# Kernel tuning notes

Measured on AMD Instinct MI355X. Metric: run time of the kernel, lower is better.

Reference implementation:

```python
import jax, jax.numpy as jnp
import numpy as np

BN_EPS = 1e-5
NEG = -9e15
ALPHA = 0.2  # LeakyReLU slope


def _gat(src, tgt, adj_mask, W, a, num_heads):
    # src: [M, H*D] source features, tgt: [N, H*D], adj_mask: [N, M] (>0 means edge)
    N, M = tgt.shape[0], src.shape[0]
    D = tgt.shape[1] // num_heads
    S = (src @ W.T).reshape(M, num_heads, D)   # W(source)
    T = (tgt @ W.T).reshape(N, num_heads, D)   # W(target)
    # concat([t_i, s_j]) . a[h] == t_i . a[h,:D] + s_j . a[h,D:]
    et = jnp.einsum('nhd,hd->hn', T, a[:, :D])  # [H, N]
    es = jnp.einsum('mhd,hd->hm', S, a[:, D:])  # [H, M]
    e = et[:, :, None] + es[:, None, :]          # [H, N, M]
    e = jnp.where(e >= 0, e, ALPHA * e)          # LeakyReLU
    e = jnp.where(adj_mask[None, :, :] > 0, e, NEG)
    attn = jax.nn.softmax(e, axis=-1)            # over source nodes
    out = jnp.einsum('hnm,mhd->nhd', attn, S)    # [N, H, D]
    return out.reshape(N, num_heads * D)


def _bn_eval(x, gamma, beta):
    # eval-mode BatchNorm1d with running_mean=0, running_var=1
    return x * (gamma / jnp.sqrt(1.0 + BN_EPS)) + beta


def setup_inputs() -> dict:
    key = jax.random.key(0)
    ks = jax.random.split(key, 12)
    N, M, H, HD = 4096, 2048, 8, 256
    D = HD // H
    c_features = jax.random.normal(ks[0], (N, HD), dtype=jnp.float32)
    d_features = jax.random.normal(ks[1], (M, HD), dtype=jnp.float32)
    cd_adj = jax.random.randint(ks[2], (N, M), 0, 2, dtype=jnp.int32)
    sc = 1.0 / np.sqrt(HD)
    c_W = jax.random.normal(ks[3], (HD, HD), dtype=jnp.float32) * sc
    d_W = jax.random.normal(ks[4], (HD, HD), dtype=jnp.float32) * sc
    sa = np.sqrt(2.0 / (H + 2 * D))  # xavier_normal_ for [H, 2D]
    c_a = jax.random.normal(ks[5], (H, 2 * D), dtype=jnp.float32) * sa
    d_a = jax.random.normal(ks[6], (H, 2 * D), dtype=jnp.float32) * sa
    c_bn_gamma = jnp.ones((HD,), dtype=jnp.float32)
    c_bn_beta = jnp.zeros((HD,), dtype=jnp.float32)
    d_bn_gamma = jnp.ones((HD,), dtype=jnp.float32)
    d_bn_beta = jnp.zeros((HD,), dtype=jnp.float32)
    return dict(c_features=c_features, d_features=d_features, cd_adj=cd_adj,
                c_W=c_W, c_a=c_a, d_W=d_W, d_a=d_a,
                c_bn_gamma=c_bn_gamma, c_bn_beta=c_bn_beta,
                d_bn_gamma=d_bn_gamma, d_bn_beta=d_bn_beta)


def reference(c_features, d_features, cd_adj, c_W, c_a, d_W, d_a,
              c_bn_gamma, c_bn_beta, d_bn_gamma, d_bn_beta):
    H = 8
    c_out = _gat(d_features, c_features, cd_adj, c_W, c_a, H)
    d_out = _gat(c_features, d_features, cd_adj.T, d_W, d_a, H)
    c_out = jax.nn.relu(_bn_eval(c_out, c_bn_gamma, c_bn_beta))
    d_out = jax.nn.relu(_bn_eval(d_out, d_bn_gamma, d_bn_beta))
    # dropout is identity in eval mode
    return (c_out, d_out)
```

## Files before the change

### kernel.cpp

```cpp
#include <hip/hip_runtime.h>
#include <hip/hip_bf16.h>

#define L2E 1.4426950408889634f
#define BNF 0.99999500003749969f

typedef __attribute__((ext_vector_type(4))) float f4;
typedef __attribute__((ext_vector_type(4))) float f32x4;
typedef __attribute__((ext_vector_type(4))) int i4;
typedef __attribute__((ext_vector_type(8))) short bfrag;

__device__ __forceinline__ int cvtpk(float lo, float hi) {
  int r;
  asm("v_cvt_pk_bf16_f32 %0, %1, %2" : "=v"(r) : "v"(lo), "v"(hi));
  return r;
}

#define MFMA16(a, b, c) __builtin_amdgcn_mfma_f32_16x16x32_bf16(a, b, c, 0, 0, 0)

__global__ __launch_bounds__(256) void prep1(
    const float* __restrict__ c_feat, const float* __restrict__ d_feat,
    const float* __restrict__ c_W, const float* __restrict__ d_W,
    const float* __restrict__ c_a, const float* __restrict__ d_a,
    const int* __restrict__ adj,
    unsigned* __restrict__ adjP, unsigned* __restrict__ adjPT,
    unsigned short* __restrict__ Xb_c, unsigned short* __restrict__ Xb_d,
    unsigned short* __restrict__ Wb_c, unsigned short* __restrict__ Wb_d,
    float* __restrict__ wa_c, float* __restrict__ wa_d) {
  const int b = blockIdx.x;
  const int t = threadIdx.x;
  if (b < 2048) {
    __shared__ int s[64][65];
    const int m0 = (b & 31) * 64, n0 = (b >> 5) * 64;
#pragma unroll
    for (int i = 0; i < 4; ++i) {
      int idx = t + i * 256;
      int r = idx >> 4, c4 = (idx & 15) * 4;
      i4 v = __builtin_nontemporal_load(
          (const i4*)(adj + (size_t)(n0 + r) * 2048 + m0 + c4));
      s[r][c4 + 0] = v.x; s[r][c4 + 1] = v.y;
      s[r][c4 + 2] = v.z; s[r][c4 + 3] = v.w;
    }
    __syncthreads();
    const int w = t >> 6, l = t & 63;
#pragma unroll 4
    for (int rr = 0; rr < 16; ++rr) {
      int r = w * 16 + rr;
      int n = n0 + r;
      unsigned long long bb = __ballot(s[r][l] != 0);
      if (l == 0) {
        size_t base = ((size_t)(n >> 4) * 64 + (m0 >> 5)) * 16 + (n & 15);
        adjP[base] = (unsigned)bb;
        adjP[base + 16] = (unsigned)(bb >> 32);
      }
    }
#pragma unroll 4
    for (int cc = 0; cc < 16; ++cc) {
      int m = m0 + w * 16 + cc;
      unsigned long long bb = __ballot(s[l][w * 16 + cc] != 0);
      if (l == 0) {
        size_t base = ((size_t)(m >> 4) * 128 + (n0 >> 5)) * 16 + (m & 15);
        adjPT[base] = (unsigned)bb;
        adjPT[base + 16] = (unsigned)(bb >> 32);
      }
    }
  } else if (b < 2880) {
    int idx = (b - 2048) * 256 + t;
    const float* S; unsigned short* D; int tt;
    if (idx < 65536)       { S = d_feat; D = Xb_c; tt = idx; }
    else if (idx < 196608) { S = c_feat; D = Xb_d; tt = idx - 65536; }
    else if (idx < 204800) { S = c_W;    D = Wb_c; tt = idx - 196608; }
    else                   { S = d_W;    D = Wb_d; tt = idx - 204800; }
    int l = tt & 63, kt = (tt >> 6) & 7, tile = tt >> 9;
    int row = tile * 16 + (l & 15);
    int col = kt * 32 + (l >> 4) * 8;
    const float* sp = S + (size_t)row * 256 + col;
    f4 v0 = *(const f4*)sp;
    f4 v1 = *(const f4*)(sp + 4);
    uint4 u;
    u.x = (unsigned)cvtpk(v0.x, v0.y);
    u.y = (unsigned)cvtpk(v0.z, v0.w);
    u.z = (unsigned)cvtpk(v1.x, v1.y);
    u.w = (unsigned)cvtpk(v1.z, v1.w);
    *(uint4*)(D + (size_t)tt * 8) = u;
  } else {
    int idx = (b - 2880) * 256 + t;
    bool cs = idx < 2048;
    int i2 = idx & 2047;
    int h = i2 >> 8, k = i2 & 255;
    const float* W = cs ? c_W : d_W;
    const float* a = cs ? c_a : d_a;
    float s = 0.f;
#pragma unroll 8
    for (int d = 0; d < 32; ++d)
      s = fmaf(a[h * 64 + d], W[(size_t)(h * 32 + d) * 256 + k], s);
    (cs ? wa_c : wa_d)[i2] = s * L2E;
  }
}

__global__ __launch_bounds__(64) void gemm2(
    const unsigned short* __restrict__ Xb_c, const unsigned short* __restrict__ Wb_c,
    const unsigned short* __restrict__ Xb_d, const unsigned short* __restrict__ Wb_d,
    const float* __restrict__ c_a, const float* __restrict__ d_a,
    unsigned short* __restrict__ Sbt_c, unsigned short* __restrict__ Sbt_d,
    float* __restrict__ es2t_c, float* __restrict__ es2t_d,
    const float* __restrict__ c_feat, const float* __restrict__ d_feat,
    const float* __restrict__ wa_c, const float* __restrict__ wa_d,
    float* __restrict__ et2_c, float* __restrict__ et2_d) {
  const int b = blockIdx.x;
  if (b < 768) {
    const bool cs = b < 256;
    const int bb = cs ? b : b - 256;
    const int rt = bb >> 1, half = bb & 1;
    const unsigned short* Xb = cs ? Xb_c : Xb_d;
    const unsigned short* Wb = cs ? Wb_c : Wb_d;
    const float* av = cs ? c_a : d_a;
    unsigned short* Sbt = cs ? Sbt_c : Sbt_d;
    float* es2t = cs ? es2t_c : es2t_d;
    const int Mrows = cs ? 2048 : 4096;
    const int l = threadIdx.x;
    const int g = l >> 4, c16 = l & 15;
    bfrag afr[8];
#pragma unroll
    for (int kt = 0; kt < 8; ++kt)
      afr[kt] = *(const bfrag*)(Xb + ((size_t)(rt * 8 + kt) * 64 + l) * 8);
    float esacc[4] = {};
#pragma unroll
    for (int c8 = 0; c8 < 8; ++c8) {
      const int cht = half * 8 + c8;
      f32x4 acc = {0.f, 0.f, 0.f, 0.f};
#pragma unroll
      for (int kt = 0; kt < 8; ++kt) {
        bfrag wfr = *(const bfrag*)(Wb + ((size_t)(cht * 8 + kt) * 64 + l) * 8);
        acc = MFMA16(afr[kt], wfr, acc);
      }
      const int mtb = rt * 2 + (g >> 1);
      size_t soff = (((size_t)cht * (Mrows >> 3) + mtb) * 16 + c16) * 8 + (g & 1) * 4;
      uint2 u;
      u.x = (unsigned)cvtpk(acc[0], acc[1]);
      u.y = (unsigned)cvtpk(acc[2], acc[3]);
      *(uint2*)(Sbt + soff) = u;
      const int h = cht >> 1, sub = cht & 1;
      const float aw = av[h * 64 + 32 + sub * 16 + c16];
      if (sub == 0) {
#pragma unroll
        for (int i = 0; i < 4; ++i) esacc[i] = acc[i] * aw;
      } else {
#pragma unroll
        for (int i = 0; i < 4; ++i) esacc[i] = fmaf(acc[i], aw, esacc[i]);
#pragma unroll
        for (int i = 0; i < 4; ++i) {
          esacc[i] += __shfl_xor(esacc[i], 1);
          esacc[i] += __shfl_xor(esacc[i], 2);
          esacc[i] += __shfl_xor(esacc[i], 4);
          esacc[i] += __shfl_xor(esacc[i], 8);
        }
        if (c16 == 0) {
          f4 o = {esacc[0] * L2E, esacc[1] * L2E, esacc[2] * L2E, esacc[3] * L2E};
          *(f4*)(es2t + (size_t)h * Mrows + rt * 16 + g * 4) = o;
        }
      }
    }
  } else {
    int idx = (b - 768) * 64 + threadIdx.x;
    bool cs = idx < 32768;
    int i2 = cs ? idx : idx - 32768;
    const float* X = cs ? c_feat : d_feat;
    const float* wa = cs ? wa_c : wa_d;
    float* et2 = cs ? et2_c : et2_d;
    int r = i2 >> 3, h = i2 & 7;
    const float* xp = X + (size_t)r * 256;
    const float* ap = wa + h * 256;
    float s = 0.f;
#pragma unroll 16
    for (int k = 0; k < 256; k += 4) {
      f4 xv = *(const f4*)(xp + k);
      f4 av = *(const f4*)(ap + k);
      s = fmaf(xv.x, av.x, s); s = fmaf(xv.y, av.y, s);
      s = fmaf(xv.z, av.z, s); s = fmaf(xv.w, av.w, s);
    }
    et2[i2] = s;
  }
}

__device__ __forceinline__ bfrag make_pfrag2(float et, f4 e0, f4 e1,
                                             unsigned bits) {
  float xv[8] = {e0.x, e0.y, e0.z, e0.w, e1.x, e1.y, e1.z, e1.w};
  float p[8];
#pragma unroll
  for (int e = 0; e < 8; ++e) {
    float x = et + xv[e];
    x = fmaxf(x, 0.2f * x);
    float pe = __builtin_amdgcn_exp2f(x);
    p[e] = ((bits >> e) & 1u) ? pe : 0.f;
  }
  union { bfrag v; int i[4]; } u;
#pragma unroll
  for (int e = 0; e < 4; ++e) u.i[e] = cvtpk(p[2 * e], p[2 * e + 1]);
  return u.v;
}

template <int FINAL, int SWZ, int CHT>
__global__ __launch_bounds__(256) void fused_attn(
    const float* __restrict__ et2_c, const float* __restrict__ es2t_c,
    const unsigned* __restrict__ adjP, const unsigned short* __restrict__ Sbt_c,
    float* __restrict__ pnum_c, float* __restrict__ pden_c,
    const float* __restrict__ et2_d, const float* __restrict__ es2t_d,
    const unsigned* __restrict__ adjPT, const unsigned short* __restrict__ Sbt_d,
    float* __restrict__ pnum_d, float* __restrict__ pden_d,
    float* __restrict__ out,
    const float* __restrict__ gc, const float* __restrict__ bc,
    const float* __restrict__ gd, const float* __restrict__ bd,
    int NBC, int CH_C, int CH_D) {
  const int b = blockIdx.x;
  bool cs; int chunk, tile;
  if (SWZ) {
    const int r = b & 7;
    if (r < 4) { cs = true;  chunk = r >> 1; tile = (b >> 3) + (r & 1) * 128; }
    else       { cs = false; chunk = r - 4;  tile = b >> 3; }
  } else {
    cs = b < NBC;
    const int bb = cs ? b : b - NBC;
    tile = cs ? (bb & 255) : (bb & 127);
    chunk = cs ? (bb >> 8) : (bb >> 7);
  }
  const int n0 = tile * 16;
  const int M = cs ? 2048 : 4096;
  const int ROWS = cs ? 4096 : 2048;
  const int CH = CHT ? CHT : (cs ? CH_C : CH_D);
  const float* et2 = cs ? et2_c : et2_d;
  const float* es2t = cs ? es2t_c : es2t_d;
  const unsigned* adjPk = cs ? adjP : adjPT;
  const unsigned short* Sbt = cs ? Sbt_c : Sbt_d;
  float* pnum = cs ? pnum_c : pnum_d;
  float* pden = cs ? pden_c : pden_d;
  const float* bng = cs ? gc : gd;
  const float* bnb = cs ? bc : bd;
  float* outp = cs ? out : out + (size_t)4096 * 256;

  const int mstart = chunk * CH;
  const int mend = mstart + CH;
  const int Mw = M >> 5;
  const int tid = threadIdx.x;
  const int w = tid >> 6, l = tid & 63;
  const int g = l >> 4, c16 = l & 15;
  const int hA = w * 2, hB = w * 2 + 1;
  const int row = n0 + c16;
  const float etA = et2[row * 8 + hA];
  const float etB = et2[row * 8 + hB];
  const int Mt16 = M * 16;
  const int lane_off = g * 128 + c16 * 8;
  const unsigned short* pA0 = Sbt + (size_t)(hA * 2) * Mt16 + lane_off;
  const unsigned short* pA1 = pA0 + Mt16;
  const unsigned short* pB0 = Sbt + (size_t)(hB * 2) * Mt16 + lane_off;
  const unsigned short* pB1 = pB0 + Mt16;
  const unsigned* adjt = adjPk + (size_t)tile * Mw * 16 + c16;
  const float* esArow = es2t + (size_t)hA * M;
  const float* esBrow = es2t + (size_t)hB * M;
  f32x4 accA0 = {0.f, 0.f, 0.f, 0.f}, accA1 = accA0, denA = accA0;
  f32x4 accB0 = accA0, accB1 = accA0, denB = accA0;
  union { bfrag v; int i[4]; } uo;
#pragma unroll
  for (int e = 0; e < 4; ++e) uo.i[e] = 0x3F803F80;
  const bfrag ones = uo.v;

  auto body = [&](int m0) {
    const unsigned w0 = adjt[(m0 >> 5) * 16];
    const unsigned w1 = adjt[(m0 >> 5) * 16 + 16];
    const int moa = m0 + g * 8;
    const int i8 = (m0 >> 3) * 128;
    f4 eA0 = *(const f4*)(esArow + moa);
    f4 eA1 = *(const f4*)(esArow + moa + 4);
    f4 eB0 = *(const f4*)(esBrow + moa);
    f4 eB1 = *(const f4*)(esBrow + moa + 4);
    f4 fA0 = *(const f4*)(esArow + moa + 32);
    f4 fA1 = *(const f4*)(esArow + moa + 36);
    f4 fB0 = *(const f4*)(esBrow + moa + 32);
    f4 fB1 = *(const f4*)(esBrow + moa + 36);
    bfrag bA0a = *(const bfrag*)(pA0 + i8);
    bfrag bA1a = *(const bfrag*)(pA1 + i8);
    bfrag bB0a = *(const bfrag*)(pB0 + i8);
    bfrag bB1a = *(const bfrag*)(pB1 + i8);
    bfrag bA0b = *(const bfrag*)(pA0 + i8 + 512);
    bfrag bA1b = *(const bfrag*)(pA1 + i8 + 512);
    bfrag bB0b = *(const bfrag*)(pB0 + i8 + 512);
    bfrag bB1b = *(const bfrag*)(pB1 + i8 + 512);
    const unsigned bits0 = (w0 >> (g * 8)) & 0xffu;
    const unsigned bits1 = (w1 >> (g * 8)) & 0xffu;
    bfrag aA = make_pfrag2(etA, eA0, eA1, bits0);
    bfrag aB = make_pfrag2(etB, eB0, eB1, bits0);
    accA0 = MFMA16(aA, bA0a, accA0);
    accA1 = MFMA16(aA, bA1a, accA1);
    denA  = MFMA16(aA, ones, denA);
    accB0 = MFMA16(aB, bB0a, accB0);
    accB1 = MFMA16(aB, bB1a, accB1);
    denB  = MFMA16(aB, ones, denB);
    bfrag cA = make_pfrag2(etA, fA0, fA1, bits1);
    bfrag cB = make_pfrag2(etB, fB0, fB1, bits1);
    accA0 = MFMA16(cA, bA0b, accA0);
    accA1 = MFMA16(cA, bA1b, accA1);
    denA  = MFMA16(cA, ones, denA);
    accB0 = MFMA16(cB, bB0b, accB0);
    accB1 = MFMA16(cB, bB1b, accB1);
    denB  = MFMA16(cB, ones, denB);
  };

  if (CHT) {
#pragma unroll 1
    for (int mm = 0; mm < CHT; mm += 512) {
#pragma unroll
      for (int it = 0; it < 8; ++it)
        body(mstart + mm + it * 64);
    }
  } else {
    for (int m0 = mstart; m0 < mend; m0 += 64)
      body(m0);
  }

#define EPILOGUE(acc0, acc1, den, h)                                          \
  {                                                                           \
    const int c0 = (h) * 32 + c16, c1 = (h) * 32 + 16 + c16;                  \
    if (FINAL) {                                                              \
      const float g0 = bng[c0] * BNF, b0 = bnb[c0];                           \
      const float g1 = bng[c1] * BNF, b1 = bnb[c1];                           \
      _Pragma("unroll") for (int i = 0; i < 4; ++i) {                         \
        float rs = 1.f / fmaxf(den[i], 1e-30f);                               \
        float* op = outp + (size_t)(n0 + g * 4 + i) * 256;                    \
        op[c0] = fmaxf(fmaf(acc0[i] * rs, g0, b0), 0.f);                      \
        op[c1] = fmaxf(fmaf(acc1[i] * rs, g1, b1), 0.f);                      \
      }                                                                       \
    } else {                                                                  \
      _Pragma("unroll") for (int i = 0; i < 4; ++i) {                         \
        size_t rr = (size_t)chunk * ROWS + n0 + g * 4 + i;                    \
        pnum[rr * 256 + c0] = acc0[i];                                        \
        pnum[rr * 256 + c1] = acc1[i];                                        \
        if (c16 == 0) pden[rr * 8 + (h)] = den[i];                            \
      }                                                                       \
    }                                                                         \
  }
  EPILOGUE(accA0, accA1, denA, hA)
  EPILOGUE(accB0, accB1, denB, hB)
#undef EPILOGUE
}

__global__ __launch_bounds__(256) void finalize_k(
    const float* __restrict__ pnum_c, const float* __restrict__ pden_c,
    const float* __restrict__ pnum_d, const float* __restrict__ pden_d,
    float* __restrict__ out,
    const float* __restrict__ gc, const float* __restrict__ bc,
    const float* __restrict__ gd, const float* __restrict__ bd,
    int cc_c, int cc_d) {
  const int b = blockIdx.x;
  const bool cs = b < 1024;
  const int idx = (cs ? b : b - 1024) * 256 + threadIdx.x;
  const int rows = cs ? 4096 : 2048;
  const int cc = cs ? cc_c : cc_d;
  const float* pnum = cs ? pnum_c : pnum_d;
  const float* pden = cs ? pden_c : pden_d;
  const float* bng = cs ? gc : gd;
  const float* bnb = cs ? bc : bd;
  float* outp = cs ? out : out + (size_t)4096 * 256;
  int r = idx >> 6, c4 = (idx & 63) * 4;
  int h = c4 >> 5;
  f4 num = {0.f, 0.f, 0.f, 0.f};
  float den = 0.f;
  for (int c = 0; c < cc; ++c) {
    size_t rr = (size_t)c * rows + r;
    num += __builtin_nontemporal_load((const f4*)(pnum + rr * 256 + c4));
    den += __builtin_nontemporal_load(pden + rr * 8 + h);
  }
  float rs = 1.f / fmaxf(den, 1e-30f);
  f4 gm = *(const f4*)(bng + c4);
  f4 bb = *(const f4*)(bnb + c4);
  f4 o;
  o.x = fmaxf(fmaf(num.x * rs, gm.x * BNF, bb.x), 0.f);
  o.y = fmaxf(fmaf(num.y * rs, gm.y * BNF, bb.y), 0.f);
  o.z = fmaxf(fmaf(num.z * rs, gm.z * BNF, bb.z), 0.f);
  o.w = fmaxf(fmaf(num.w * rs, gm.w * BNF, bb.w), 0.f);
  *(f4*)(outp + (size_t)r * 256 + c4) = o;
}

extern "C" void kernel_launch(void* const* d_in, const int* in_sizes, int n_in,
                              void* d_out, int out_size, void* d_ws, size_t ws_size,
                              hipStream_t stream) {
  const float* c_feat = (const float*)d_in[0];
  const float* d_feat = (const float*)d_in[1];
  const int*   adj    = (const int*)d_in[2];
  const float* c_W    = (const float*)d_in[3];
  const float* c_a    = (const float*)d_in[4];
  const float* d_W    = (const float*)d_in[5];
  const float* d_a    = (const float*)d_in[6];
  const float* c_bn_g = (const float*)d_in[7];
  const float* c_bn_b = (const float*)d_in[8];
  const float* d_bn_g = (const float*)d_in[9];
  const float* d_bn_b = (const float*)d_in[10];
  float* out = (float*)d_out;

  char* w = (char*)d_ws;
  size_t off = 0;
  auto take = [&](size_t bytes) -> char* {
    char* p = w + off;
    off += (bytes + 255) & ~(size_t)255;
    return p;
  };
  unsigned short* Sbt_c = (unsigned short*)take(256 * 2048 * 2);
  unsigned short* Sbt_d = (unsigned short*)take(256 * 4096 * 2);
  unsigned short* Xb_c  = (unsigned short*)take(2048 * 256 * 2);
  unsigned short* Xb_d  = (unsigned short*)take(4096 * 256 * 2);
  unsigned short* Wb_c  = (unsigned short*)take(256 * 256 * 2);
  unsigned short* Wb_d  = (unsigned short*)take(256 * 256 * 2);
  float* et2_c  = (float*)take(4096 * 8 * 4);
  float* es2t_c = (float*)take(8 * 2048 * 4);
  float* et2_d  = (float*)take(2048 * 8 * 4);
  float* es2t_d = (float*)take(8 * 4096 * 4);
  float* wa_c   = (float*)take(8 * 256 * 4);
  float* wa_d   = (float*)take(8 * 256 * 4);
  unsigned* adjP  = (unsigned*)take(4096 * 64 * 4);
  unsigned* adjPT = (unsigned*)take(2048 * 128 * 4);

  const size_t base = off;
  const size_t PC = (size_t)4096 * 256 * 4, PD = (size_t)2048 * 256 * 4;
  const size_t DC = 4096 * 8 * 4, DD = 2048 * 8 * 4;
  auto need = [&](int a, int b2) -> size_t {
    return base + (size_t)a * (PC + DC) + (size_t)b2 * (PD + DD) + 4096;
  };
  int ccc = 0, ccd = 0;
  if (ws_size >= need(2, 4))      { ccc = 2; ccd = 4; }
  else if (ws_size >= need(2, 2)) { ccc = 2; ccd = 2; }

  float* pden_c = nullptr; float* pden_d = nullptr;
  float* pnum_c = nullptr; float* pnum_d = nullptr;
  if (ccc) {
    pden_c = (float*)take((size_t)ccc * DC);
    pden_d = (float*)take((size_t)ccd * DD);
    pnum_c = (float*)take((size_t)ccc * PC);
    pnum_d = (float*)take((size_t)ccd * PD);
  }

  dim3 blk(256);
  prep1<<<2896, blk, 0, stream>>>(c_feat, d_feat, c_W, d_W, c_a, d_a, adj,
                                  adjP, adjPT, Xb_c, Xb_d, Wb_c, Wb_d,
                                  wa_c, wa_d);
  gemm2<<<1536, dim3(64), 0, stream>>>(Xb_c, Wb_c, Xb_d, Wb_d, c_a, d_a,
                                       Sbt_c, Sbt_d, es2t_c, es2t_d,
                                       c_feat, d_feat, wa_c, wa_d,
                                       et2_c, et2_d);

  if (ccc == 2 && ccd == 4) {
    fused_attn<0, 1, 1024><<<1024, blk, 0, stream>>>(
        et2_c, es2t_c, adjP, Sbt_c, pnum_c, pden_c,
        et2_d, es2t_d, adjPT, Sbt_d, pnum_d, pden_d,
        nullptr, c_bn_g, c_bn_b, d_bn_g, d_bn_b,
        512, 1024, 1024);
    finalize_k<<<1536, blk, 0, stream>>>(pnum_c, pden_c, pnum_d, pden_d, out,
                                         c_bn_g, c_bn_b, d_bn_g, d_bn_b, ccc, ccd);
  } else if (ccc) {
    fused_attn<0, 0, 0><<<256 * ccc + 128 * ccd, blk, 0, stream>>>(
        et2_c, es2t_c, adjP, Sbt_c, pnum_c, pden_c,
        et2_d, es2t_d, adjPT, Sbt_d, pnum_d, pden_d,
        nullptr, c_bn_g, c_bn_b, d_bn_g, d_bn_b,
        256 * ccc, 2048 / ccc, 4096 / ccd);
    finalize_k<<<1536, blk, 0, stream>>>(pnum_c, pden_c, pnum_d, pden_d, out,
                                         c_bn_g, c_bn_b, d_bn_g, d_bn_b, ccc, ccd);
  } else {
    fused_attn<1, 0, 0><<<384, blk, 0, stream>>>(
        et2_c, es2t_c, adjP, Sbt_c, nullptr, nullptr,
        et2_d, es2t_d, adjPT, Sbt_d, nullptr, nullptr,
        out, c_bn_g, c_bn_b, d_bn_g, d_bn_b, 256, 2048, 4096);
  }
}
```

Measured before the change: 77.99 us.

## Replace global split-M partials with in-block LDS reduction across waves

```diff
diff --git a/kernel.cpp b/kernel.cpp
--- a/kernel.cpp
+++ b/kernel.cpp
@@ -199,51 +199,35 @@
   return u.v;
 }
 
-template <int FINAL, int SWZ, int CHT>
-__global__ __launch_bounds__(256) void fused_attn(
+__global__ __launch_bounds__(256) void fused_rs(
     const float* __restrict__ et2_c, const float* __restrict__ es2t_c,
     const unsigned* __restrict__ adjP, const unsigned short* __restrict__ Sbt_c,
-    float* __restrict__ pnum_c, float* __restrict__ pden_c,
     const float* __restrict__ et2_d, const float* __restrict__ es2t_d,
     const unsigned* __restrict__ adjPT, const unsigned short* __restrict__ Sbt_d,
-    float* __restrict__ pnum_d, float* __restrict__ pden_d,
     float* __restrict__ out,
     const float* __restrict__ gc, const float* __restrict__ bc,
-    const float* __restrict__ gd, const float* __restrict__ bd,
-    int NBC, int CH_C, int CH_D) {
+    const float* __restrict__ gd, const float* __restrict__ bd) {
+  __shared__ __align__(16) f4 red[4][6][64];
   const int b = blockIdx.x;
-  bool cs; int chunk, tile;
-  if (SWZ) {
-    const int r = b & 7;
-    if (r < 4) { cs = true;  chunk = r >> 1; tile = (b >> 3) + (r & 1) * 128; }
-    else       { cs = false; chunk = r - 4;  tile = b >> 3; }
-  } else {
-    cs = b < NBC;
-    const int bb = cs ? b : b - NBC;
-    tile = cs ? (bb & 255) : (bb & 127);
-    chunk = cs ? (bb >> 8) : (bb >> 7);
-  }
+  const bool cs = b < 1024;
+  const int bb = cs ? b : b - 1024;
+  const int hp = bb & 3, tile = bb >> 2;
   const int n0 = tile * 16;
   const int M = cs ? 2048 : 4096;
-  const int ROWS = cs ? 4096 : 2048;
-  const int CH = CHT ? CHT : (cs ? CH_C : CH_D);
   const float* et2 = cs ? et2_c : et2_d;
   const float* es2t = cs ? es2t_c : es2t_d;
   const unsigned* adjPk = cs ? adjP : adjPT;
   const unsigned short* Sbt = cs ? Sbt_c : Sbt_d;
-  float* pnum = cs ? pnum_c : pnum_d;
-  float* pden = cs ? pden_c : pden_d;
   const float* bng = cs ? gc : gd;
   const float* bnb = cs ? bc : bd;
   float* outp = cs ? out : out + (size_t)4096 * 256;
 
-  const int mstart = chunk * CH;
-  const int mend = mstart + CH;
   const int Mw = M >> 5;
+  const int Mq = M >> 2;
   const int tid = threadIdx.x;
   const int w = tid >> 6, l = tid & 63;
   const int g = l >> 4, c16 = l & 15;
-  const int hA = w * 2, hB = w * 2 + 1;
+  const int hA = hp * 2, hB = hp * 2 + 1;
   const int row = n0 + c16;
   const float etA = et2[row * 8 + hA];
   const float etB = et2[row * 8 + hB];
@@ -304,22 +288,27 @@
     denB  = MFMA16(cB, ones, denB);
   };
 
-  if (CHT) {
+  const int mstart = w * Mq;
 #pragma unroll 1
-    for (int mm = 0; mm < CHT; mm += 512) {
-#pragma unroll
-      for (int it = 0; it < 8; ++it)
-        body(mstart + mm + it * 64);
-    }
-  } else {
-    for (int m0 = mstart; m0 < mend; m0 += 64)
-      body(m0);
-  }
-
+  for (int mm = 0; mm < Mq; mm += 512) {
+#pragma unroll
+    for (int it = 0; it < 8; ++it)
+      body(mstart + mm + it * 64);
+  }
+
+  red[w][0][l] = accA0; red[w][1][l] = accA1; red[w][2][l] = denA;
+  red[w][3][l] = accB0; red[w][4][l] = accB1; red[w][5][l] = denB;
+  __syncthreads();
+  if (w == 0) {
+    f4 rA0 = red[0][0][l] + red[1][0][l] + red[2][0][l] + red[3][0][l];
+    f4 rA1 = red[0][1][l] + red[1][1][l] + red[2][1][l] + red[3][1][l];
+    f4 rdA = red[0][2][l] + red[1][2][l] + red[2][2][l] + red[3][2][l];
+    f4 rB0 = red[0][3][l] + red[1][3][l] + red[2][3][l] + red[3][3][l];
+    f4 rB1 = red[0][4][l] + red[1][4][l] + red[2][4][l] + red[3][4][l];
+    f4 rdB = red[0][5][l] + red[1][5][l] + red[2][5][l] + red[3][5][l];
 #define EPILOGUE(acc0, acc1, den, h)                                          \
-  {                                                                           \
-    const int c0 = (h) * 32 + c16, c1 = (h) * 32 + 16 + c16;                  \
-    if (FINAL) {                                                              \
+    {                                                                         \
+      const int c0 = (h) * 32 + c16, c1 = (h) * 32 + 16 + c16;                \
       const float g0 = bng[c0] * BNF, b0 = bnb[c0];                           \
       const float g1 = bng[c1] * BNF, b1 = bnb[c1];                           \
       _Pragma("unroll") for (int i = 0; i < 4; ++i) {                         \
@@ -328,55 +317,11 @@
         op[c0] = fmaxf(fmaf(acc0[i] * rs, g0, b0), 0.f);                      \
         op[c1] = fmaxf(fmaf(acc1[i] * rs, g1, b1), 0.f);                      \
       }                                                                       \
-    } else {                                                                  \
-      _Pragma("unroll") for (int i = 0; i < 4; ++i) {                         \
-        size_t rr = (size_t)chunk * ROWS + n0 + g * 4 + i;                    \
-        pnum[rr * 256 + c0] = acc0[i];                                        \
-        pnum[rr * 256 + c1] = acc1[i];                                        \
-        if (c16 == 0) pden[rr * 8 + (h)] = den[i];                            \
-      }                                                                       \
-    }                                                                         \
-  }
-  EPILOGUE(accA0, accA1, denA, hA)
-  EPILOGUE(accB0, accB1, denB, hB)
+    }
+    EPILOGUE(rA0, rA1, rdA, hA)
+    EPILOGUE(rB0, rB1, rdB, hB)
 #undef EPILOGUE
-}
-
-__global__ __launch_bounds__(256) void finalize_k(
-    const float* __restrict__ pnum_c, const float* __restrict__ pden_c,
-    const float* __restrict__ pnum_d, const float* __restrict__ pden_d,
-    float* __restrict__ out,
-    const float* __restrict__ gc, const float* __restrict__ bc,
-    const float* __restrict__ gd, const float* __restrict__ bd,
-    int cc_c, int cc_d) {
-  const int b = blockIdx.x;
-  const bool cs = b < 1024;
-  const int idx = (cs ? b : b - 1024) * 256 + threadIdx.x;
-  const int rows = cs ? 4096 : 2048;
-  const int cc = cs ? cc_c : cc_d;
-  const float* pnum = cs ? pnum_c : pnum_d;
-  const float* pden = cs ? pden_c : pden_d;
-  const float* bng = cs ? gc : gd;
-  const float* bnb = cs ? bc : bd;
-  float* outp = cs ? out : out + (size_t)4096 * 256;
-  int r = idx >> 6, c4 = (idx & 63) * 4;
-  int h = c4 >> 5;
-  f4 num = {0.f, 0.f, 0.f, 0.f};
-  float den = 0.f;
-  for (int c = 0; c < cc; ++c) {
-    size_t rr = (size_t)c * rows + r;
-    num += __builtin_nontemporal_load((const f4*)(pnum + rr * 256 + c4));
-    den += __builtin_nontemporal_load(pden + rr * 8 + h);
-  }
-  float rs = 1.f / fmaxf(den, 1e-30f);
-  f4 gm = *(const f4*)(bng + c4);
-  f4 bb = *(const f4*)(bnb + c4);
-  f4 o;
-  o.x = fmaxf(fmaf(num.x * rs, gm.x * BNF, bb.x), 0.f);
-  o.y = fmaxf(fmaf(num.y * rs, gm.y * BNF, bb.y), 0.f);
-  o.z = fmaxf(fmaf(num.z * rs, gm.z * BNF, bb.z), 0.f);
-  o.w = fmaxf(fmaf(num.w * rs, gm.w * BNF, bb.w), 0.f);
-  *(f4*)(outp + (size_t)r * 256 + c4) = o;
+  }
 }
 
 extern "C" void kernel_launch(void* const* d_in, const int* in_sizes, int n_in,
@@ -416,25 +361,7 @@
   float* wa_d   = (float*)take(8 * 256 * 4);
   unsigned* adjP  = (unsigned*)take(4096 * 64 * 4);
   unsigned* adjPT = (unsigned*)take(2048 * 128 * 4);
-
-  const size_t base = off;
-  const size_t PC = (size_t)4096 * 256 * 4, PD = (size_t)2048 * 256 * 4;
-  const size_t DC = 4096 * 8 * 4, DD = 2048 * 8 * 4;
-  auto need = [&](int a, int b2) -> size_t {
-    return base + (size_t)a * (PC + DC) + (size_t)b2 * (PD + DD) + 4096;
-  };
-  int ccc = 0, ccd = 0;
-  if (ws_size >= need(2, 4))      { ccc = 2; ccd = 4; }
-  else if (ws_size >= need(2, 2)) { ccc = 2; ccd = 2; }
-
-  float* pden_c = nullptr; float* pden_d = nullptr;
-  float* pnum_c = nullptr; float* pnum_d = nullptr;
-  if (ccc) {
-    pden_c = (float*)take((size_t)ccc * DC);
-    pden_d = (float*)take((size_t)ccd * DD);
-    pnum_c = (float*)take((size_t)ccc * PC);
-    pnum_d = (float*)take((size_t)ccd * PD);
-  }
+  (void)off; (void)ws_size;
 
   dim3 blk(256);
   prep1<<<2896, blk, 0, stream>>>(c_feat, d_feat, c_W, d_W, c_a, d_a, adj,
@@ -444,27 +371,7 @@
                                        Sbt_c, Sbt_d, es2t_c, es2t_d,
                                        c_feat, d_feat, wa_c, wa_d,
                                        et2_c, et2_d);
-
-  if (ccc == 2 && ccd == 4) {
-    fused_attn<0, 1, 1024><<<1024, blk, 0, stream>>>(
-        et2_c, es2t_c, adjP, Sbt_c, pnum_c, pden_c,
-        et2_d, es2t_d, adjPT, Sbt_d, pnum_d, pden_d,
-        nullptr, c_bn_g, c_bn_b, d_bn_g, d_bn_b,
-        512, 1024, 1024);
-    finalize_k<<<1536, blk, 0, stream>>>(pnum_c, pden_c, pnum_d, pden_d, out,
-                                         c_bn_g, c_bn_b, d_bn_g, d_bn_b, ccc, ccd);
-  } else if (ccc) {
-    fused_attn<0, 0, 0><<<256 * ccc + 128 * ccd, blk, 0, stream>>>(
-        et2_c, es2t_c, adjP, Sbt_c, pnum_c, pden_c,
-        et2_d, es2t_d, adjPT, Sbt_d, pnum_d, pden_d,
-        nullptr, c_bn_g, c_bn_b, d_bn_g, d_bn_b,
-        256 * ccc, 2048 / ccc, 4096 / ccd);
-    finalize_k<<<1536, blk, 0, stream>>>(pnum_c, pden_c, pnum_d, pden_d, out,
-                                         c_bn_g, c_bn_b, d_bn_g, d_bn_b, ccc, ccd);
-  } else {
-    fused_attn<1, 0, 0><<<384, blk, 0, stream>>>(
-        et2_c, es2t_c, adjP, Sbt_c, nullptr, nullptr,
-        et2_d, es2t_d, adjPT, Sbt_d, nullptr, nullptr,
-        out, c_bn_g, c_bn_b, d_bn_g, d_bn_b, 256, 2048, 4096);
-  }
-}
+  fused_rs<<<1536, blk, 0, stream>>>(et2_c, es2t_c, adjP, Sbt_c,
+                                     et2_d, es2t_d, adjPT, Sbt_d,
+                                     out, c_bn_g, c_bn_b, d_bn_g, d_bn_b);
+}
```

Result: slower. 104.9 us (+34.5%).
